# Optimization experiments

Measured on AMD Instinct MI355X. Metric: run time of the kernel, lower is better.

Reference implementation:

```python
import jax, jax.numpy as jnp
import numpy as np

G = 16       # groups
GRID = 25    # hardcoded self.grid
EPS = 1e-5   # BatchNorm eps


def _gconv(x, w, pad):
    # x: (B, Cin, H, W), w: (Cout, Cin//G, kh, kw); grouped conv, stride 1
    return jax.lax.conv_general_dilated(
        x, w, window_strides=(1, 1), padding=[(pad, pad), (pad, pad)],
        feature_group_count=G)


def _bn_relu(h, g, b, m, v):
    # h: (G, B, C, H, W); per-group-instance BN params: (G, C). Inference BN.
    scale = (g / jnp.sqrt(v + EPS))[:, None, :, None, None]
    return jax.nn.relu((h - m[:, None, :, None, None]) * scale + b[:, None, :, None, None])


def setup_inputs() -> dict:
    key = jax.random.key(0)
    ks = jax.random.split(key, 11)
    B, C, H, W = 2, 256, 24, 24
    AC = GRID * C  # 6400 affinity channels
    return {
        "x":  jax.random.normal(ks[0], (B, C, H, W), jnp.float32),
        "W1": jax.random.normal(ks[1], (G, C, C // G, 3, 3), jnp.float32) * 0.05,
        "g1": jax.random.uniform(ks[2], (G, C), jnp.float32, 0.5, 1.5),
        "b1": jax.random.normal(ks[3], (G, C), jnp.float32) * 0.1,
        "m1": jax.random.normal(ks[4], (G, C), jnp.float32) * 0.1,
        "v1": jax.random.uniform(ks[5], (G, C), jnp.float32, 0.5, 1.5),
        "W2": jax.random.normal(ks[6], (G, AC, C // G, 1, 1), jnp.float32) * 0.05,
        "g2": jax.random.uniform(ks[7], (G, AC), jnp.float32, 0.5, 1.5),
        "b2": jax.random.normal(ks[8], (G, AC), jnp.float32) * 0.1,
        "m2": jax.random.normal(ks[9], (G, AC), jnp.float32) * 0.1,
        "v2": jax.random.uniform(ks[10], (G, AC), jnp.float32, 0.5, 1.5),
    }


def reference(x, W1, g1, b1, m1, v1, W2, g2, b2, m2, v2):
    B, C, H, W = x.shape
    Cg = C // G
    # 16 independent grouped 3x3 convs over the same input, batched via vmap
    h1 = jax.vmap(lambda w: _gconv(x, w, 1))(W1)          # (G, B, C, H, W)
    h1 = _bn_relu(h1, g1, b1, m1, v1)
    # grouped 1x1 conv with padding=1 (faithful to source -> spatial grows to H+2, W+2)
    a = jax.vmap(lambda h, w: _gconv(h, w, 1))(h1, W2)    # (G, B, 25C, H+2, W+2)
    a = _bn_relu(a, g2, b2, m2, v2)
    pooled = a.mean(axis=(-2, -1))                        # adaptive avg pool -> (G, B, 25C)
    xv = pooled.reshape(G, B, G, GRID * Cg)               # (G, B, G, 25*Cg)
    aff = jnp.einsum('ibkm,iblm->ibkl', xv, xv)           # (G, B, G, G) = theta @ phi
    idx = jnp.arange(G)
    aff_i = aff[idx, :, idx, :] / G                       # aff[:, i], /N  -> (G, B, G)
    ex = h1.reshape(G, B, G, Cg * H * W)
    # torch.matmul((B,G), (B,G,M)) broadcasts 2-D lhs -> (B, B, M); kept faithfully
    z = jnp.einsum('ipk,iqkm->ipqm', aff_i, ex)           # (G, B, B, Cg*H*W)
    z = z.reshape(G, B, B, Cg, H, W).transpose(1, 0, 2, 3, 4, 5)
    return z.reshape(B, G * B * Cg, H, W)                 # (B, B*C, H, W)
```

## Files before the change

kernel.cpp:

```cpp
#include <hip/hip_runtime.h>
#include <hip/hip_bf16.h>


typedef __attribute__((ext_vector_type(8))) short short8;
typedef __attribute__((ext_vector_type(4))) short short4v;
typedef __attribute__((ext_vector_type(4))) float f32x4;

static __device__ __forceinline__ short f2bf(float x) {
    unsigned u = __float_as_uint(x);
    unsigned r = (u + 0x7fffu + ((u >> 16) & 1u)) >> 16;
    return (short)r;
}

__global__ __launch_bounds__(256) void k12_fused(
    const float* __restrict__ xin,
    const float* __restrict__ W1,
    const float* __restrict__ g1, const float* __restrict__ b1,
    const float* __restrict__ m1, const float* __restrict__ v1,
    const float* __restrict__ W2,
    const float* __restrict__ g2, const float* __restrict__ b2,
    const float* __restrict__ m2, const float* __restrict__ v2,
    float* __restrict__ h1f,
    float* __restrict__ pooled)
{
    __shared__ __align__(16) char smem[43840];
    short* xs    = (short*)smem;
    short* wA    = (short*)(smem + 33696);
    short* hsb   = (short*)smem;
    short* wlb   = (short*)(smem + 23040);
    float* psum  = (float*)(smem + 35840);
    float* bias2 = (float*)(smem + 42240);
    __shared__ float scale1[16], bias1[16];

    int bid = blockIdx.x;
    int i = bid >> 5, b = (bid >> 4) & 1, g = bid & 15;
    int t = threadIdx.x;

    int* xz = (int*)xs;
    for (int idx = t; idx < 27*26*12; idx += 256) xz[idx] = 0;
    if (t < 16) {
        int c = i*256 + g*16 + t;
        float sc = g1[c] * rsqrtf(v1[c] + 1e-5f);
        scale1[t] = sc;
        bias1[t]  = b1[c] - m1[c] * sc;
    }
    __syncthreads();

    const float* xb = &xin[(b*256 + g*16)*576];
    for (int idx = t; idx < 9216; idx += 256) {
        int ci = idx / 576; int s = idx - ci*576;
        int y = s / 24; int x = s - y*24;
        xs[((y+1)*26 + (x+1))*24 + ci] = f2bf(xb[idx]);
    }
    const float* wb = &W1[(i*256 + g*16)*144];
    for (int idx = t; idx < 2560; idx += 256) {
        int kk = idx >> 9, rem = idx & 511, co = rem >> 5, k = rem & 31;
        int tap = 2*kk + (k >> 4), ci = k & 15;
        float val = (tap < 9) ? wb[co*144 + ci*9 + tap] * scale1[co] : 0.f;
        wA[(kk*16 + co)*40 + k] = f2bf(val);
    }
    __syncthreads();

    int l = t & 63, w = t >> 6;
    int quad = l >> 4, col = l & 15;
    {
        int ci0 = (quad & 1) * 8;
        short8 afr[5];
#pragma unroll
        for (int kk = 0; kk < 5; kk++)
            afr[kk] = *(const short8*)&wA[(kk*16 + col)*40 + quad*8];
        f32x4 cb1 = *(const f32x4*)&bias1[quad*4];

        const int offE[5] = {0, 48, 648, 1248, 1296};
        const int offO[5] = {24, 624, 672, 1272, 1872};
        int off[5];
#pragma unroll
        for (int kk = 0; kk < 5; kk++) off[kk] = (quad >= 2) ? offO[kk] : offE[kk];

        f32x4 dreg[9];
#pragma unroll 3
        for (int tt = 0; tt < 9; tt++) {
            int s = (w*9 + tt)*16 + col;
            int y = s / 24; int x = s - y*24;
            int base = (y*26 + x)*24 + ci0;
            f32x4 acc = cb1;
#pragma unroll
            for (int kk = 0; kk < 5; kk++) {
                short8 bf = *(const short8*)&xs[base + off[kk]];
                acc = __builtin_amdgcn_mfma_f32_16x16x32_bf16(afr[kk], bf, acc, 0, 0, 0);
            }
#pragma unroll
            for (int r = 0; r < 4; r++) acc[r] = fmaxf(acc[r], 0.f);
            dreg[tt] = acc;
        }
        __syncthreads();

        float* hout = &h1f[((i*2 + b)*256 + g*16)*576];
#pragma unroll
        for (int tt = 0; tt < 9; tt++) {
            int s = (w*9 + tt)*16 + col;
            f32x4 acc = dreg[tt];
            unsigned p0 = (unsigned)(unsigned short)f2bf(acc[0]) |
                          ((unsigned)(unsigned short)f2bf(acc[1]) << 16);
            unsigned p1 = (unsigned)(unsigned short)f2bf(acc[2]) |
                          ((unsigned)(unsigned short)f2bf(acc[3]) << 16);
            uint2 pk = {p0, p1};
            *(uint2*)&hsb[s*20 + quad*4] = pk;
#pragma unroll
            for (int r = 0; r < 4; r++)
                hout[(quad*4 + r)*576 + s] = acc[r];
        }
    }

    for (int m = t; m < 400; m += 256) {
        int o = i*6400 + g*400 + m;
        float s2 = g2[o] * rsqrtf(v2[o] + 1e-5f);
        bias2[m] = b2[o] - m2[o] * s2;
        const float4* wr = (const float4*)&W2[o*16];
#pragma unroll
        for (int q = 0; q < 4; q++) {
            float4 wv = wr[q];
            wlb[m*16 + q*4 + 0] = f2bf(wv.x * s2);
            wlb[m*16 + q*4 + 1] = f2bf(wv.y * s2);
            wlb[m*16 + q*4 + 2] = f2bf(wv.z * s2);
            wlb[m*16 + q*4 + 3] = f2bf(wv.w * s2);
        }
    }
    __syncthreads();

    int half = l >> 4;
    {
        short8 bfr[9];
#pragma unroll
        for (int u = 0; u < 9; u++) {
            if (l < 32) {
                const short* p = &hsb[((w*9 + u)*16 + col)*20 + half*8];
                short4v lo = *(const short4v*)p;
                short4v hi = *(const short4v*)(p + 4);
                short8 f; f[0]=lo.x; f[1]=lo.y; f[2]=lo.z; f[3]=lo.w;
                          f[4]=hi.x; f[5]=hi.y; f[6]=hi.z; f[7]=hi.w;
                bfr[u] = f;
            } else {
                bfr[u] = (short8)0;
            }
        }

        for (int mt = 0; mt < 25; mt++) {
            short8 af = (short8)0;
            if (l < 32)
                af = *(const short8*)&wlb[(mt*16 + col)*16 + half*8];

            f32x4 cb = *(const f32x4*)&bias2[mt*16 + half*4];

            f32x4 d[9];
#pragma unroll
            for (int u = 0; u < 9; u++)
                d[u] = __builtin_amdgcn_mfma_f32_16x16x32_bf16(af, bfr[u], cb, 0, 0, 0);

            float p0=0.f, p1=0.f, p2=0.f, p3=0.f;
#pragma unroll
            for (int u = 0; u < 9; u++) {
                p0 += fmaxf(d[u][0], 0.f);
                p1 += fmaxf(d[u][1], 0.f);
                p2 += fmaxf(d[u][2], 0.f);
                p3 += fmaxf(d[u][3], 0.f);
            }
#pragma unroll
            for (int msk = 1; msk < 16; msk <<= 1) {
                p0 += __shfl_xor(p0, msk);
                p1 += __shfl_xor(p1, msk);
                p2 += __shfl_xor(p2, msk);
                p3 += __shfl_xor(p3, msk);
            }
            if (col == 0) {
                f32x4 pv = {p0, p1, p2, p3};
                *(f32x4*)&psum[w*400 + mt*16 + half*4] = pv;
            }
        }
    }
    __syncthreads();

    const float inv = 1.f / 676.f;
    for (int m = t; m < 400; m += 256) {
        float s = psum[0*400+m] + psum[1*400+m] + psum[2*400+m] + psum[3*400+m];
        float be = bias2[m];
        pooled[(i*2+b)*6400 + g*400 + m] = (s + 100.f * fmaxf(be, 0.f)) * inv;
    }
}

__global__ __launch_bounds__(256) void k3_aff(const float* __restrict__ pooled,
                                              float* __restrict__ aff)
{
    __shared__ float th[400];
    __shared__ float parts[256];
    int bid = blockIdx.x;
    int i = bid >> 1;
    int t = threadIdx.x;
    const float* pb = &pooled[bid*6400];
    for (int idx = t; idx < 400; idx += 256) th[idx] = pb[i*400 + idx];
    __syncthreads();
    int l = t >> 4, p = t & 15;
    float sum = 0.f;
    const float* pl = &pb[l*400];
    for (int m = p*25; m < p*25 + 25; m++) sum = fmaf(th[m], pl[m], sum);
    parts[t] = sum;
    __syncthreads();
    if (t < 16) {
        float s = 0.f;
        for (int pp = 0; pp < 16; pp++) s += parts[t*16 + pp];
        aff[bid*16 + t] = s * (1.f/16.f);
    }
}

__global__ __launch_bounds__(256) void k4_out(const float* __restrict__ h1f,
                                              const float* __restrict__ aff,
                                              float* __restrict__ out)
{
    __shared__ float a0[16], a1[16];
    int bid = blockIdx.x;
    int i = bid >> 5, q = (bid >> 4) & 1, cg = bid & 15;
    int t = threadIdx.x;
    if (t < 16) a0[t] = aff[(i*2+0)*16 + t];
    else if (t < 32) a1[t-16] = aff[(i*2+1)*16 + (t-16)];
    __syncthreads();
    const float* hb = &h1f[((i*2+q)*256 + cg)*576];
    int ch = i*32 + q*16 + cg;
    for (int s = t; s < 576; s += 256) {
        float acc0 = 0.f, acc1 = 0.f;
#pragma unroll
        for (int k = 0; k < 16; k++) {
            float v = hb[k*9216 + s];
            acc0 = fmaf(a0[k], v, acc0);
            acc1 = fmaf(a1[k], v, acc1);
        }
        out[ch*576 + s]         = acc0;
        out[(512 + ch)*576 + s] = acc1;
    }
}

extern "C" void kernel_launch(void* const* d_in, const int* in_sizes, int n_in,
                              void* d_out, int out_size, void* d_ws, size_t ws_size,
                              hipStream_t stream)
{
    const float* x  = (const float*)d_in[0];
    const float* W1 = (const float*)d_in[1];
    const float* g1 = (const float*)d_in[2];
    const float* b1 = (const float*)d_in[3];
    const float* m1 = (const float*)d_in[4];
    const float* v1 = (const float*)d_in[5];
    const float* W2 = (const float*)d_in[6];
    const float* g2 = (const float*)d_in[7];
    const float* b2 = (const float*)d_in[8];
    const float* m2 = (const float*)d_in[9];
    const float* v2 = (const float*)d_in[10];

    float* h1f    = (float*)d_ws;
    float* pooled = h1f + 16*2*256*576;
    float* aff    = pooled + 16*2*6400;

    float* out = (float*)d_out;

    hipLaunchKernelGGL(k12_fused, dim3(512), dim3(256), 0, stream,
                       x, W1, g1, b1, m1, v1, W2, g2, b2, m2, v2, h1f, pooled);
    hipLaunchKernelGGL(k3_aff,    dim3(32),  dim3(256), 0, stream,
                       pooled, aff);
    hipLaunchKernelGGL(k4_out,    dim3(512), dim3(256), 0, stream,
                       h1f, aff, out);
}
```

Baseline: 129.2 us.

## Split 1x1 conv output tiles across waves instead of spatial positions

Reassigns the second-stage MFMA work so each wave owns a subset of the 25 output-channel tiles and loops over all 36 spatial tiles, swapping operand roles so channels land on the lane dimension. This removes the per-tile 16-lane butterfly shuffle reduction, the shared-memory partial-sum buffer, the extra barrier and the final cross-wave combine loop, and it also shrinks the shared-memory allocation. The cost is uneven load: waves get 7 or 6 tiles out of 25. Spatial fragments are now reread from LDS for every tile instead of held in registers, and the MFMA chain per tile is longer and serial.

```diff
diff --git a/kernel.cpp b/kernel.cpp
--- a/kernel.cpp
+++ b/kernel.cpp
@@ -23,13 +23,12 @@
     float* __restrict__ h1f,
     float* __restrict__ pooled)
 {
-    __shared__ __align__(16) char smem[43840];
+    __shared__ __align__(16) char smem[40096];
     short* xs    = (short*)smem;
     short* wA    = (short*)(smem + 33696);
     short* hsb   = (short*)smem;
     short* wlb   = (short*)(smem + 23040);
-    float* psum  = (float*)(smem + 35840);
-    float* bias2 = (float*)(smem + 42240);
+    float* bias2 = (float*)(smem + 35840);
     __shared__ float scale1[16], bias1[16];
 
     int bid = blockIdx.x;
@@ -62,13 +61,13 @@
     __syncthreads();
 
     int l = t & 63, w = t >> 6;
-    int quad = l >> 4, col = l & 15;
+    int quad = l >> 4, rc = l & 15;
     {
         int ci0 = (quad & 1) * 8;
         short8 afr[5];
 #pragma unroll
         for (int kk = 0; kk < 5; kk++)
-            afr[kk] = *(const short8*)&wA[(kk*16 + col)*40 + quad*8];
+            afr[kk] = *(const short8*)&wA[(kk*16 + rc)*40 + quad*8];
         f32x4 cb1 = *(const f32x4*)&bias1[quad*4];
 
         const int offE[5] = {0, 48, 648, 1248, 1296};
@@ -80,7 +79,7 @@
         f32x4 dreg[9];
 #pragma unroll 3
         for (int tt = 0; tt < 9; tt++) {
-            int s = (w*9 + tt)*16 + col;
+            int s = (w*9 + tt)*16 + rc;
             int y = s / 24; int x = s - y*24;
             int base = (y*26 + x)*24 + ci0;
             f32x4 acc = cb1;
@@ -98,7 +97,7 @@
         float* hout = &h1f[((i*2 + b)*256 + g*16)*576];
 #pragma unroll
         for (int tt = 0; tt < 9; tt++) {
-            int s = (w*9 + tt)*16 + col;
+            int s = (w*9 + tt)*16 + rc;
             f32x4 acc = dreg[tt];
             unsigned p0 = (unsigned)(unsigned short)f2bf(acc[0]) |
                           ((unsigned)(unsigned short)f2bf(acc[1]) << 16);
@@ -128,63 +127,41 @@
     }
     __syncthreads();
 
-    int half = l >> 4;
     {
-        short8 bfr[9];
-#pragma unroll
-        for (int u = 0; u < 9; u++) {
-            if (l < 32) {
-                const short* p = &hsb[((w*9 + u)*16 + col)*20 + half*8];
-                short4v lo = *(const short4v*)p;
-                short4v hi = *(const short4v*)(p + 4);
-                short8 f; f[0]=lo.x; f[1]=lo.y; f[2]=lo.z; f[3]=lo.w;
-                          f[4]=hi.x; f[5]=hi.y; f[6]=hi.z; f[7]=hi.w;
-                bfr[u] = f;
-            } else {
-                bfr[u] = (short8)0;
+        int q8 = (quad & 1) * 8;
+        const float inv = 1.f / 676.f;
+        for (int mt = w; mt < 25; mt += 4) {
+            int m0 = mt*16;
+            short8 wf = (short8)0;
+            if (l < 32)
+                wf = *(const short8*)&wlb[(m0 + rc)*16 + q8];
+            float be = bias2[m0 + rc];
+            f32x4 cb = {be, be, be, be};
+
+            f32x4 accv = {0.f, 0.f, 0.f, 0.f};
+#pragma unroll 4
+            for (int s0 = 0; s0 < 36; s0++) {
+                short8 af = (short8)0;
+                if (l < 32) {
+                    const short* p = &hsb[(s0*16 + rc)*20 + q8];
+                    short4v lo = *(const short4v*)p;
+                    short4v hi = *(const short4v*)(p + 4);
+                    short8 f; f[0]=lo.x; f[1]=lo.y; f[2]=lo.z; f[3]=lo.w;
+                              f[4]=hi.x; f[5]=hi.y; f[6]=hi.z; f[7]=hi.w;
+                    af = f;
+                }
+                f32x4 d = __builtin_amdgcn_mfma_f32_16x16x32_bf16(af, wf, cb, 0, 0, 0);
+#pragma unroll
+                for (int r = 0; r < 4; r++)
+                    accv[r] += fmaxf(d[r], 0.f);
             }
-        }
-
-        for (int mt = 0; mt < 25; mt++) {
-            short8 af = (short8)0;
-            if (l < 32)
-                af = *(const short8*)&wlb[(mt*16 + col)*16 + half*8];
-
-            f32x4 cb = *(const f32x4*)&bias2[mt*16 + half*4];
-
-            f32x4 d[9];
-#pragma unroll
-            for (int u = 0; u < 9; u++)
-                d[u] = __builtin_amdgcn_mfma_f32_16x16x32_bf16(af, bfr[u], cb, 0, 0, 0);
-
-            float p0=0.f, p1=0.f, p2=0.f, p3=0.f;
-#pragma unroll
-            for (int u = 0; u < 9; u++) {
-                p0 += fmaxf(d[u][0], 0.f);
-                p1 += fmaxf(d[u][1], 0.f);
-                p2 += fmaxf(d[u][2], 0.f);
-                p3 += fmaxf(d[u][3], 0.f);
-            }
-#pragma unroll
-            for (int msk = 1; msk < 16; msk <<= 1) {
-                p0 += __shfl_xor(p0, msk);
-                p1 += __shfl_xor(p1, msk);
-                p2 += __shfl_xor(p2, msk);
-                p3 += __shfl_xor(p3, msk);
-            }
-            if (col == 0) {
-                f32x4 pv = {p0, p1, p2, p3};
-                *(f32x4*)&psum[w*400 + mt*16 + half*4] = pv;
-            }
-        }
-    }
-    __syncthreads();
-
-    const float inv = 1.f / 676.f;
-    for (int m = t; m < 400; m += 256) {
-        float s = psum[0*400+m] + psum[1*400+m] + psum[2*400+m] + psum[3*400+m];
-        float be = bias2[m];
-        pooled[(i*2+b)*6400 + g*400 + m] = (s + 100.f * fmaxf(be, 0.f)) * inv;
+            float a = (accv[0] + accv[1]) + (accv[2] + accv[3]);
+            a += __shfl_xor(a, 16);
+            a += __shfl_xor(a, 32);
+            if (l < 16)
+                pooled[(i*2+b)*6400 + g*400 + m0 + l] =
+                    (a + 100.f * fmaxf(be, 0.f)) * inv;
+        }
     }
 }
 
```

Result: no change. 129.7 us (+0.3%).
